# Performance work log

Measured on AMD Instinct MI355X. Metric: run time of the kernel, lower is better.

Reference implementation:

```python
import jax, jax.numpy as jnp
import numpy as np

N = 45056      # 2048 instances * 22 machines
E = 720896     # avg degree 16
FEA = 60       # max_num*6
HID = 256
MACH = 22
NEG_SLOPE = 0.01


def setup_inputs() -> dict:
    key = jax.random.key(0)
    ks = jax.random.split(key, 20)
    x = jax.random.normal(ks[0], (N, FEA), dtype=jnp.float32)
    edge_index = jax.random.randint(ks[1], (2, E), 0, N, dtype=jnp.int64)
    edge_weight = jax.random.uniform(ks[2], (E,), dtype=jnp.float32)

    def lin(k, fan_in, fan_out):
        s = 1.0 / np.sqrt(fan_in)
        kw, kb = jax.random.split(k)
        W = jax.random.uniform(kw, (fan_in, fan_out), minval=-s, maxval=s, dtype=jnp.float32)
        b = jax.random.uniform(kb, (fan_out,), minval=-s, maxval=s, dtype=jnp.float32)
        return W, b

    W1, b1 = lin(ks[3], FEA, HID)
    W2, b2 = lin(ks[4], HID, HID)
    mlp_in = MACH * (HID + FEA)  # 6952
    Wf0, bf0 = lin(ks[5], mlp_in, HID)
    Wf1, bf1 = lin(ks[6], HID, HID)
    Wf2, bf2 = lin(ks[7], HID, HID)
    Wo, bo = lin(ks[8], HID, 4)
    return {"x": x, "edge_index": edge_index, "edge_weight": edge_weight,
            "W1": W1, "b1": b1, "W2": W2, "b2": b2,
            "Wf0": Wf0, "bf0": bf0, "Wf1": Wf1, "bf1": bf1,
            "Wf2": Wf2, "bf2": bf2, "Wo": Wo, "bo": bo}


def _gcn_conv(h, W, b, row, col, norm, n):
    # h' = scatter_add(norm * (hW)[row] -> col) + b   (PyG GCNConv)
    hw = h @ W                                  # [N, out]
    msg = hw[row] * norm[:, None]               # [E+N, out]
    out = jax.ops.segment_sum(msg, col, num_segments=n)
    return out + b


def reference(x, edge_index, edge_weight, W1, b1, W2, b2,
              Wf0, bf0, Wf1, bf1, Wf2, bf2, Wo, bo):
    n = x.shape[0]
    # gcn_norm with self-loops (fill_value=1.0), symmetric normalization
    loop = jnp.arange(n, dtype=edge_index.dtype)
    row = jnp.concatenate([edge_index[0], loop])
    col = jnp.concatenate([edge_index[1], loop])
    ew = jnp.concatenate([edge_weight, jnp.ones((n,), dtype=edge_weight.dtype)])
    deg = jax.ops.segment_sum(ew, col, num_segments=n)
    dinv = jnp.where(deg > 0, jax.lax.rsqrt(jnp.maximum(deg, 1e-12)), 0.0)
    norm = dinv[row] * ew * dinv[col]

    h = _gcn_conv(x, W1, b1, row, col, norm, n)
    h = jax.nn.leaky_relu(h, NEG_SLOPE)
    # dropout p=0.5 is identity in eval mode
    h = _gcn_conv(h, W2, b2, row, col, norm, n)
    h = jax.nn.leaky_relu(h, NEG_SLOPE)

    h = jnp.concatenate([h, x], axis=1)         # [N, HID+FEA]
    flat = h.reshape(n // MACH, -1)             # [B, 22*(HID+FEA)]

    z = jax.nn.leaky_relu(flat @ Wf0 + bf0, NEG_SLOPE)
    z = jax.nn.leaky_relu(z @ Wf1 + bf1, NEG_SLOPE)
    z = jax.nn.leaky_relu(z @ Wf2 + bf2, NEG_SLOPE)
    return z @ Wo + bo                           # [B, 4]
```

## Files before the change

kernel.cpp:

```cpp
#include <hip/hip_runtime.h>
#include <stdint.h>

#define FEA 60
#define HID 256
#define MACH 22
#define PERM 316
#define PERM2 320
#define FLATP2 (MACH * PERM2)
#define NEG 0.01f

typedef __bf16 bf16x8 __attribute__((ext_vector_type(8)));
typedef float f32x4 __attribute__((ext_vector_type(4)));

__device__ __forceinline__ float bf2f(uint16_t u) {
    return __uint_as_float(((uint32_t)u) << 16);
}
__device__ __forceinline__ uint16_t f2bf(float f) {
    uint32_t x = __float_as_uint(f);
    return (uint16_t)((x + 0x7fffu + ((x >> 16) & 1u)) >> 16);
}
__device__ __forceinline__ int load_idx(const void* p, long i, int i64) {
    return i64 ? (int)((const long long*)p)[i] : ((const int*)p)[i];
}
__device__ __forceinline__ float load_w(const void* p, long i, int isbf) {
    return isbf ? bf2f(((const uint16_t*)p)[i]) : ((const float*)p)[i];
}

__global__ void k_detect(const uint32_t* ew_w, const uint32_t* ei_w, int* flags) {
    __shared__ int c15, onz;
    if (threadIdx.x == 0) { c15 = 0; onz = 0; }
    __syncthreads();
    int a = 0, b = 0;
    for (int i = threadIdx.x; i < 1024; i += 256) {
        if (ew_w[i] & 0x8000u) a++;
        if (ei_w[2 * i + 1] != 0u) b++;
    }
    atomicAdd(&c15, a); atomicAdd(&onz, b);
    __syncthreads();
    if (threadIdx.x == 0) {
        flags[0] = (c15 <= 100) ? 1 : 0;
        flags[1] = (onz < 8) ? 1 : 0;
    }
}

struct Cvt8 {
    const void* src[8];
    float* dst[8];
    long prefix[9];
    int cnt;
};

__global__ void k_cvt_f32(Cvt8 a, const int* flags) {
    int isbf = flags[0];
    long total = a.prefix[a.cnt];
    for (long i = (long)blockIdx.x * blockDim.x + threadIdx.x; i < total;
         i += (long)gridDim.x * blockDim.x) {
        int t = 0;
        while (i >= a.prefix[t + 1]) t++;
        long j = i - a.prefix[t];
        a.dst[t][j] = isbf ? bf2f(((const uint16_t*)a.src[t])[j])
                           : ((const float*)a.src[t])[j];
    }
}

__global__ void k_cvt_x(const void* src, uint16_t* dst, int n, const int* flags) {
    int isbf = flags[0];
    long total = (long)n * 64;
    for (long i = (long)blockIdx.x * blockDim.x + threadIdx.x; i < total;
         i += (long)gridDim.x * blockDim.x) {
        int col = (int)(i & 63);
        long row = i >> 6;
        uint16_t v = 0;
        if (col < FEA) {
            long s = row * FEA + col;
            v = isbf ? ((const uint16_t*)src)[s] : f2bf(((const float*)src)[s]);
        }
        dst[i] = v;
    }
}

__global__ void k_transp(const void* W, uint16_t* Wt, int K, int Kpad, const int* flags) {
    __shared__ uint16_t s[64][65];
    int isbf = flags[0];
    int k0 = blockIdx.x * 64, n0 = blockIdx.y * 64;
    int t = threadIdx.x;
#pragma unroll
    for (int i = 0; i < 16; i++) {
        int idx = t + i * 256;
        int kk = idx >> 6, nn = idx & 63;
        int k = k0 + kk;
        uint16_t v = 0;
        if (k < K) {
            long off = (long)k * HID + n0 + nn;
            v = isbf ? ((const uint16_t*)W)[off] : f2bf(((const float*)W)[off]);
        }
        s[kk][nn] = v;
    }
    __syncthreads();
#pragma unroll
    for (int i = 0; i < 16; i++) {
        int idx = t + i * 256;
        int nn = idx >> 6, kk = idx & 63;
        Wt[(long)(n0 + nn) * Kpad + k0 + kk] = s[kk][nn];
    }
}

__global__ void k_transp_wf0(const void* W, uint16_t* Wt, const int* flags) {
    __shared__ uint16_t s[64][65];
    int isbf = flags[0];
    int g0 = blockIdx.x * 64, n0 = blockIdx.y * 64;
    int t = threadIdx.x;
#pragma unroll
    for (int i = 0; i < 16; i++) {
        int idx = t + i * 256;
        int gg = idx >> 6, nn = idx & 63;
        int gk = g0 + gg;
        int m = gk / PERM2;
        int k2 = gk - m * PERM2;
        uint16_t v = 0;
        if (k2 < PERM) {
            long off = (long)(m * PERM + k2) * HID + n0 + nn;
            v = isbf ? ((const uint16_t*)W)[off] : f2bf(((const float*)W)[off]);
        }
        s[gg][nn] = v;
    }
    __syncthreads();
#pragma unroll
    for (int i = 0; i < 16; i++) {
        int idx = t + i * 256;
        int nn = idx >> 6, gg = idx & 63;
        Wt[(long)(n0 + nn) * FLATP2 + g0 + gg] = s[gg][nn];
    }
}

__global__ void k_init(int* count, int n) {
    int i = blockIdx.x * blockDim.x + threadIdx.x;
    if (i < n) count[i] = 0;
}

__global__ void k_count(const void* ei, int E, int* count, int* rank, const int* flags) {
    int e = blockIdx.x * blockDim.x + threadIdx.x;
    if (e >= E) return;
    int c = load_idx(ei, (long)E + e, flags[1]);
    rank[e] = atomicAdd(&count[c], 1);
}

__global__ void k_scan1(const int* count, int* rowptr, int* bsum, int n) {
    __shared__ int sd[1024];
    int i = blockIdx.x * 1024 + threadIdx.x;
    int v = (i < n) ? count[i] : 0;
    sd[threadIdx.x] = v;
    __syncthreads();
    for (int off = 1; off < 1024; off <<= 1) {
        int t = (threadIdx.x >= (unsigned)off) ? sd[threadIdx.x - off] : 0;
        __syncthreads();
        sd[threadIdx.x] += t;
        __syncthreads();
    }
    if (i < n) rowptr[i] = sd[threadIdx.x] - v;
    if (threadIdx.x == 1023) bsum[blockIdx.x] = sd[1023];
}

__global__ void k_scan2(int* bsum, int* boffs, int* rowptr, int nb, int n) {
    int acc = 0;
    for (int i = 0; i < nb; i++) { boffs[i] = acc; acc += bsum[i]; }
    rowptr[n] = acc;
}

__global__ void k_scan3(int* rowptr, const int* boffs, int n) {
    int i = blockIdx.x * 1024 + threadIdx.x;
    if (i < n) rowptr[i] += boffs[blockIdx.x];
}

__global__ void k_fill(const void* ei, const void* ew, const int* rowptr, const int* rank,
                       int* adj_src, float* adj_w, int E, const int* flags) {
    int e = blockIdx.x * blockDim.x + threadIdx.x;
    if (e >= E) return;
    int i64 = flags[1];
    int r = load_idx(ei, e, i64);
    int c = load_idx(ei, (long)E + e, i64);
    float w = load_w(ew, e, flags[0]);
    int pos = rowptr[c] + rank[e];
    adj_src[pos] = r;
    adj_w[pos] = w;
}

__global__ void k_rowsum(const int* rowptr, const float* adj_w, float* dinv, int n) {
    int i = blockIdx.x * blockDim.x + threadIdx.x;
    if (i >= n) return;
    int s = rowptr[i], e = rowptr[i + 1];
    double d = 1.0;
    for (int p = s; p < e; p++) d += (double)adj_w[p];
    dinv[i] = (float)(1.0 / sqrt(d));
}

__global__ __launch_bounds__(256) void k_aggx(const uint16_t* __restrict__ x64,
                                              const float* __restrict__ dinv,
                                              const int* __restrict__ rowptr,
                                              const int* __restrict__ adj_src,
                                              const float* __restrict__ adj_w,
                                              uint16_t* __restrict__ xa, int n) {
    __shared__ int ssrc[8][32];
    __shared__ float swt[8][32];
    int hwv = threadIdx.x >> 5;
    int l32 = threadIdx.x & 31;
    int node = blockIdx.x * 8 + hwv;
    if (node >= n) return;
    const uint32_t* xu = (const uint32_t*)x64;
    float di = dinv[node];
    float c2 = di * di;
    uint32_t h = xu[(long)node * 32 + l32];
    float a0 = c2 * bf2f((uint16_t)(h & 0xffff));
    float a1 = c2 * bf2f((uint16_t)(h >> 16));
    int s = rowptr[node], e = rowptr[node + 1];
    for (int base = s; base < e; base += 32) {
        int m = e - base; if (m > 32) m = 32;
        if (l32 < m) {
            int s0 = adj_src[base + l32];
            ssrc[hwv][l32] = s0;
            swt[hwv][l32] = adj_w[base + l32] * dinv[s0] * di;
        }
        for (int t = 0; t < m; t++) {
            int src = ssrc[hwv][t];
            float w = swt[hwv][t];
            uint32_t v = xu[(long)src * 32 + l32];
            a0 += w * bf2f((uint16_t)(v & 0xffff));
            a1 += w * bf2f((uint16_t)(v >> 16));
        }
    }
    ((uint32_t*)xa)[(long)node * 32 + l32] =
        (uint32_t)f2bf(a0) | ((uint32_t)f2bf(a1) << 16);
}

__global__ __launch_bounds__(256) void k_aggb(const uint16_t* __restrict__ hw,
                                              const float* __restrict__ dinv,
                                              const int* __restrict__ rowptr,
                                              const int* __restrict__ adj_src,
                                              const float* __restrict__ adj_w,
                                              const float* __restrict__ bias,
                                              uint16_t* __restrict__ out, int n) {
    __shared__ int ssrc[4][64];
    __shared__ float swt[4][64];
    int wv = threadIdx.x >> 6;
    int lane = threadIdx.x & 63;
    int node = blockIdx.x * 4 + wv;
    if (node >= n) return;
    const uint2* hw2 = (const uint2*)hw;
    float di = dinv[node];
    float c2 = di * di;
    uint2 h = hw2[(long)node * 64 + lane];
    float a0 = c2 * bf2f((uint16_t)(h.x & 0xffff));
    float a1 = c2 * bf2f((uint16_t)(h.x >> 16));
    float a2 = c2 * bf2f((uint16_t)(h.y & 0xffff));
    float a3 = c2 * bf2f((uint16_t)(h.y >> 16));
    int s = rowptr[node], e = rowptr[node + 1];
    for (int base = s; base < e; base += 64) {
        int m = e - base; if (m > 64) m = 64;
        if (lane < m) {
            int s0 = adj_src[base + lane];
            ssrc[wv][lane] = s0;
            swt[wv][lane] = adj_w[base + lane] * dinv[s0] * di;
        }
        for (int t = 0; t < m; t++) {
            int src = ssrc[wv][t];
            float w = swt[wv][t];
            uint2 v = hw2[(long)src * 64 + lane];
            a0 += w * bf2f((uint16_t)(v.x & 0xffff));
            a1 += w * bf2f((uint16_t)(v.x >> 16));
            a2 += w * bf2f((uint16_t)(v.y & 0xffff));
            a3 += w * bf2f((uint16_t)(v.y >> 16));
        }
    }
    float4 b4 = ((const float4*)bias)[lane];
    a0 += b4.x; a1 += b4.y; a2 += b4.z; a3 += b4.w;
    a0 = a0 > 0.f ? a0 : NEG * a0;
    a1 = a1 > 0.f ? a1 : NEG * a1;
    a2 = a2 > 0.f ? a2 : NEG * a2;
    a3 = a3 > 0.f ? a3 : NEG * a3;
    uint2 o;
    o.x = (uint32_t)f2bf(a0) | ((uint32_t)f2bf(a1) << 16);
    o.y = (uint32_t)f2bf(a2) | ((uint32_t)f2bf(a3) << 16);
    ((uint2*)out)[(long)node * 64 + lane] = o;
}

__global__ __launch_bounds__(256) void k_mgemm(const uint16_t* __restrict__ A,
                                               const uint16_t* __restrict__ Bt,
                                               float* __restrict__ part,
                                               uint16_t* __restrict__ outb,
                                               const float* __restrict__ bias,
                                               int M, int K, int Kc, int act) {
    __shared__ uint16_t As[128 * 40];
    __shared__ uint16_t Bs[128 * 40];
    int tid = threadIdx.x;
    int lane = tid & 63, wv = tid >> 6;
    int quad = lane >> 4, l15 = lane & 15;
    int row0 = blockIdx.y * 128, col0 = blockIdx.x * 128;
    int kbeg = blockIdx.z * Kc;
    int kend = kbeg + Kc; if (kend > K) kend = K;
    int arow = (wv >> 1) * 64;
    int bcol = (wv & 1) * 64;

    f32x4 acc[4][4];
#pragma unroll
    for (int i = 0; i < 4; i++)
#pragma unroll
        for (int j = 0; j < 4; j++) acc[i][j] = (f32x4){0.f, 0.f, 0.f, 0.f};

    for (int kc = kbeg; kc < kend; kc += 32) {
#pragma unroll
        for (int i = 0; i < 2; i++) {
            int idx = tid + i * 256;
            int r = idx >> 2, cq = idx & 3;
            uint4 va = *(const uint4*)(A + (long)(row0 + r) * K + kc + cq * 8);
            *(uint4*)(&As[r * 40 + cq * 8]) = va;
            uint4 vb = *(const uint4*)(Bt + (long)(col0 + r) * K + kc + cq * 8);
            *(uint4*)(&Bs[r * 40 + cq * 8]) = vb;
        }
        __syncthreads();
        bf16x8 af[4], bfr[4];
#pragma unroll
        for (int i = 0; i < 4; i++)
            af[i] = __builtin_bit_cast(bf16x8,
                *(const uint4*)(&As[(arow + i * 16 + l15) * 40 + quad * 8]));
#pragma unroll
        for (int j = 0; j < 4; j++)
            bfr[j] = __builtin_bit_cast(bf16x8,
                *(const uint4*)(&Bs[(bcol + j * 16 + l15) * 40 + quad * 8]));
#pragma unroll
        for (int i = 0; i < 4; i++)
#pragma unroll
            for (int j = 0; j < 4; j++)
                acc[i][j] = __builtin_amdgcn_mfma_f32_16x16x32_bf16(af[i], bfr[j], acc[i][j], 0, 0, 0);
        __syncthreads();
    }

#pragma unroll
    for (int i = 0; i < 4; i++)
#pragma unroll
        for (int j = 0; j < 4; j++) {
            int row = row0 + arow + i * 16 + quad * 4;
            int col = col0 + bcol + j * 16 + l15;
#pragma unroll
            for (int reg = 0; reg < 4; reg++) {
                float v = acc[i][j][reg];
                long o = (long)(row + reg) * HID + col;
                if (part) part[(long)blockIdx.z * M * HID + o] = v;
                else {
                    if (bias) v += bias[col];
                    if (act) v = v > 0.f ? v : NEG * v;
                    outb[o] = f2bf(v);
                }
            }
        }
}

__global__ __launch_bounds__(256) void k_mgemm_flat(const uint16_t* __restrict__ h2,
                                                    const uint16_t* __restrict__ x64,
                                                    const uint16_t* __restrict__ Bt,
                                                    float* __restrict__ part,
                                                    int M, int Kc) {
    __shared__ uint16_t As[128 * 40];
    __shared__ uint16_t Bs[128 * 40];
    int tid = threadIdx.x;
    int lane = tid & 63, wv = tid >> 6;
    int quad = lane >> 4, l15 = lane & 15;
    int row0 = blockIdx.y * 128, col0 = blockIdx.x * 128;
    int kbeg = blockIdx.z * Kc;
    int kend = kbeg + Kc;
    int arow = (wv >> 1) * 64;
    int bcol = (wv & 1) * 64;

    f32x4 acc[4][4];
#pragma unroll
    for (int i = 0; i < 4; i++)
#pragma unroll
        for (int j = 0; j < 4; j++) acc[i][j] = (f32x4){0.f, 0.f, 0.f, 0.f};

    for (int kc = kbeg; kc < kend; kc += 32) {
#pragma unroll
        for (int i = 0; i < 2; i++) {
            int idx = tid + i * 256;
            int r = idx >> 2, cq = idx & 3;
            int gk = kc + cq * 8;
            int m = gk / PERM2;
            int k2 = gk - m * PERM2;
            long node = (long)(row0 + r) * MACH + m;
            uint4 va = (k2 < HID)
                ? *(const uint4*)(h2 + node * HID + k2)
                : *(const uint4*)(x64 + node * 64 + (k2 - HID));
            *(uint4*)(&As[r * 40 + cq * 8]) = va;
            uint4 vb = *(const uint4*)(Bt + (long)(col0 + r) * FLATP2 + gk);
            *(uint4*)(&Bs[r * 40 + cq * 8]) = vb;
        }
        __syncthreads();
        bf16x8 af[4], bfr[4];
#pragma unroll
        for (int i = 0; i < 4; i++)
            af[i] = __builtin_bit_cast(bf16x8,
                *(const uint4*)(&As[(arow + i * 16 + l15) * 40 + quad * 8]));
#pragma unroll
        for (int j = 0; j < 4; j++)
            bfr[j] = __builtin_bit_cast(bf16x8,
                *(const uint4*)(&Bs[(bcol + j * 16 + l15) * 40 + quad * 8]));
#pragma unroll
        for (int i = 0; i < 4; i++)
#pragma unroll
            for (int j = 0; j < 4; j++)
                acc[i][j] = __builtin_amdgcn_mfma_f32_16x16x32_bf16(af[i], bfr[j], acc[i][j], 0, 0, 0);
        __syncthreads();
    }

#pragma unroll
    for (int i = 0; i < 4; i++)
#pragma unroll
        for (int j = 0; j < 4; j++) {
            int row = row0 + arow + i * 16 + quad * 4;
            int col = col0 + bcol + j * 16 + l15;
#pragma unroll
            for (int reg = 0; reg < 4; reg++)
                part[(long)blockIdx.z * M * HID + (long)(row + reg) * HID + col] = acc[i][j][reg];
        }
}

__global__ void k_reduce(const float* __restrict__ part, const float* __restrict__ bias,
                         uint16_t* __restrict__ out, int MN, int S) {
    int i = blockIdx.x * blockDim.x + threadIdx.x;
    if (i >= MN) return;
    float v = 0.f;
    for (int s = 0; s < S; s++) v += part[(long)s * MN + i];
    v += bias[i & (HID - 1)];
    v = v > 0.f ? v : NEG * v;
    out[i] = f2bf(v);
}

__global__ __launch_bounds__(256) void k_tail(const uint16_t* __restrict__ z0,
                                              const uint16_t* __restrict__ Wf1t,
                                              const float* __restrict__ bf1,
                                              const uint16_t* __restrict__ Wf2t,
                                              const float* __restrict__ bf2,
                                              const float* __restrict__ Wo,
                                              const float* __restrict__ bo,
                                              void* out, const int* flags) {
    __shared__ uint16_t z1s[16 * 256];
    __shared__ uint16_t z2s[16 * 256];
    int tid = threadIdx.x;
    int lane = tid & 63, wv = tid >> 6;
    int quad = lane >> 4, l15 = lane & 15;
    int rows0 = blockIdx.x * 16;
    int nw = wv * 64;

    {
        f32x4 acc[4];
#pragma unroll
        for (int j = 0; j < 4; j++) acc[j] = (f32x4){0.f, 0.f, 0.f, 0.f};
        for (int kc = 0; kc < HID; kc += 32) {
            bf16x8 a = __builtin_bit_cast(bf16x8,
                *(const uint4*)(z0 + (long)(rows0 + l15) * HID + kc + quad * 8));
#pragma unroll
            for (int j = 0; j < 4; j++) {
                bf16x8 b = __builtin_bit_cast(bf16x8,
                    *(const uint4*)(Wf1t + (long)(nw + j * 16 + l15) * HID + kc + quad * 8));
                acc[j] = __builtin_amdgcn_mfma_f32_16x16x32_bf16(a, b, acc[j], 0, 0, 0);
            }
        }
#pragma unroll
        for (int j = 0; j < 4; j++) {
            int col = nw + j * 16 + l15;
            float bj = bf1[col];
#pragma unroll
            for (int reg = 0; reg < 4; reg++) {
                float v = acc[j][reg] + bj;
                v = v > 0.f ? v : NEG * v;
                z1s[(quad * 4 + reg) * 256 + col] = f2bf(v);
            }
        }
    }
    __syncthreads();

    {
        f32x4 acc[4];
#pragma unroll
        for (int j = 0; j < 4; j++) acc[j] = (f32x4){0.f, 0.f, 0.f, 0.f};
        for (int kc = 0; kc < HID; kc += 32) {
            bf16x8 a = __builtin_bit_cast(bf16x8,
                *(const uint4*)(&z1s[l15 * 256 + kc + quad * 8]));
#pragma unroll
            for (int j = 0; j < 4; j++) {
                bf16x8 b = __builtin_bit_cast(bf16x8,
                    *(const uint4*)(Wf2t + (long)(nw + j * 16 + l15) * HID + kc + quad * 8));
                acc[j] = __builtin_amdgcn_mfma_f32_16x16x32_bf16(a, b, acc[j], 0, 0, 0);
            }
        }
#pragma unroll
        for (int j = 0; j < 4; j++) {
            int col = nw + j * 16 + l15;
            float bj = bf2[col];
#pragma unroll
            for (int reg = 0; reg < 4; reg++) {
                float v = acc[j][reg] + bj;
                v = v > 0.f ? v : NEG * v;
                z2s[(quad * 4 + reg) * 256 + col] = f2bf(v);
            }
        }
    }
    __syncthreads();

    if (tid < 64) {
        int r = tid >> 2, o = tid & 3;
        float acc = bo[o];
        for (int k = 0; k < HID; k++)
            acc += bf2f(z2s[r * 256 + k]) * Wo[k * 4 + o];
        long idx = (long)(rows0 + r) * 4 + o;
        if (flags[0]) ((uint16_t*)out)[idx] = f2bf(acc);
        else          ((float*)out)[idx] = acc;
    }
}

extern "C" void kernel_launch(void* const* d_in, const int* in_sizes, int n_in,
                              void* d_out, int out_size, void* d_ws, size_t ws_size,
                              hipStream_t stream) {
    const int N  = in_sizes[0] / FEA;
    const int E  = in_sizes[2];
    const int Bn = N / MACH;
    const int S0 = 11, Kc0 = FLATP2 / 11;

    char* ws = (char*)d_ws;
    size_t off = 0;
    auto alloc = [&](size_t bytes) -> char* {
        char* p = ws + off;
        off = (off + bytes + 255) & ~(size_t)255;
        return p;
    };

    int*      flags  = (int*)     alloc(64);
    uint16_t* x64    = (uint16_t*)alloc((size_t)N * 64 * 2);
    uint16_t* xa     = (uint16_t*)alloc((size_t)N * 64 * 2);
    uint16_t* W1t    = (uint16_t*)alloc((size_t)HID * 64 * 2);
    uint16_t* W2t    = (uint16_t*)alloc((size_t)HID * HID * 2);
    uint16_t* Wf0t   = (uint16_t*)alloc((size_t)HID * FLATP2 * 2);
    uint16_t* Wf1t   = (uint16_t*)alloc((size_t)HID * HID * 2);
    uint16_t* Wf2t   = (uint16_t*)alloc((size_t)HID * HID * 2);
    float*    b1     = (float*)   alloc(HID * 4);
    float*    b2     = (float*)   alloc(HID * 4);
    float*    bf0    = (float*)   alloc(HID * 4);
    float*    bf1    = (float*)   alloc(HID * 4);
    float*    bf2    = (float*)   alloc(HID * 4);
    float*    Wo     = (float*)   alloc((size_t)HID * 4 * 4);
    float*    bo     = (float*)   alloc(4 * 4);
    int*      count  = (int*)     alloc((size_t)N * 4);
    int*      rank   = (int*)     alloc((size_t)E * 4);
    int*      rowptr = (int*)     alloc((size_t)(N + 1) * 4);
    int*      bsum   = (int*)     alloc(64 * 4);
    int*      boffs  = (int*)     alloc(64 * 4);
    int*      adj_src= (int*)     alloc((size_t)E * 4);
    float*    adj_w  = (float*)   alloc((size_t)E * 4);
    float*    dinv   = (float*)   alloc((size_t)N * 4);
    uint16_t* P      = (uint16_t*)alloc((size_t)N * HID * 2);
    uint16_t* Q      = (uint16_t*)alloc((size_t)N * HID * 2);
    float*    part   = (float*)   alloc((size_t)S0 * Bn * HID * 4);
    uint16_t* z0     = (uint16_t*)alloc((size_t)Bn * HID * 2);
    (void)ws_size; (void)n_in; (void)out_size;

    k_detect<<<1, 256, 0, stream>>>((const uint32_t*)d_in[2], (const uint32_t*)d_in[1], flags);

    Cvt8 c8{};
    const void* s8[7] = { d_in[4], d_in[6], d_in[8], d_in[10], d_in[12], d_in[13], d_in[14] };
    float* d8[7] = { b1, b2, bf0, bf1, bf2, Wo, bo };
    long n8[7] = { HID, HID, HID, HID, HID, (long)HID * 4, 4 };
    c8.cnt = 7;
    c8.prefix[0] = 0;
    for (int t = 0; t < 7; t++) { c8.src[t] = s8[t]; c8.dst[t] = d8[t]; c8.prefix[t + 1] = c8.prefix[t] + n8[t]; }
    c8.prefix[8] = c8.prefix[7];
    k_cvt_f32<<<64, 256, 0, stream>>>(c8, flags);
    k_cvt_x<<<2048, 256, 0, stream>>>(d_in[0], x64, N, flags);
    k_transp<<<dim3(1, 4), 256, 0, stream>>>(d_in[3], W1t, FEA, 64, flags);
    k_transp<<<dim3(4, 4), 256, 0, stream>>>(d_in[5], W2t, HID, HID, flags);
    k_transp_wf0<<<dim3(FLATP2 / 64, 4), 256, 0, stream>>>(d_in[7], Wf0t, flags);
    k_transp<<<dim3(4, 4), 256, 0, stream>>>(d_in[9], Wf1t, HID, HID, flags);
    k_transp<<<dim3(4, 4), 256, 0, stream>>>(d_in[11], Wf2t, HID, HID, flags);

    k_init<<<(N + 255) / 256, 256, 0, stream>>>(count, N);
    k_count<<<(E + 255) / 256, 256, 0, stream>>>(d_in[1], E, count, rank, flags);
    int nb = (N + 1023) / 1024;
    k_scan1<<<nb, 1024, 0, stream>>>(count, rowptr, bsum, N);
    k_scan2<<<1, 1, 0, stream>>>(bsum, boffs, rowptr, nb, N);
    k_scan3<<<nb, 1024, 0, stream>>>(rowptr, boffs, N);
    k_fill<<<(E + 255) / 256, 256, 0, stream>>>(d_in[1], d_in[2], rowptr, rank, adj_src, adj_w, E, flags);
    k_rowsum<<<(N + 255) / 256, 256, 0, stream>>>(rowptr, adj_w, dinv, N);

    k_aggx<<<(N + 7) / 8, 256, 0, stream>>>(x64, dinv, rowptr, adj_src, adj_w, xa, N);
    k_mgemm<<<dim3(2, N / 128, 1), 256, 0, stream>>>(xa, W1t, nullptr, P, b1, N, 64, 64, 1);

    k_mgemm<<<dim3(2, N / 128, 1), 256, 0, stream>>>(P, W2t, nullptr, Q, nullptr, N, HID, HID, 0);
    k_aggb<<<(N + 3) / 4, 256, 0, stream>>>(Q, dinv, rowptr, adj_src, adj_w, b2, P, N);

    k_mgemm_flat<<<dim3(2, Bn / 128, S0), 256, 0, stream>>>(P, x64, Wf0t, part, Bn, Kc0);
    k_reduce<<<(Bn * HID + 255) / 256, 256, 0, stream>>>(part, bf0, z0, Bn * HID, S0);

    k_tail<<<Bn / 16, 256, 0, stream>>>(z0, Wf1t, bf1, Wf2t, bf2, Wo, bo, d_out, flags);
}
```

Baseline: 374.2 us.

## Fuse setup kernels, pack adjacency as uint2, widen gather loads and retune split-K

Merges several small preprocessing launches (detect+init, x and bias conversion, three weight transposes, scan2 into scan3) to cut launch overhead. Packs the CSR source index and weight into a single uint2 array and processes two edges per thread in count/fill. The aggregation kernels get 4-way unrolled gathers, and k_aggb switches to 32-lane half-waves with 16-byte loads. The split-K for the first flat GEMM changes from 11 to 8 splits with clamping. Risks include more serial prefix work in scan3 and fewer workgroups in the flat GEMM.

```diff
diff --git a/kernel.cpp b/kernel.cpp
--- a/kernel.cpp
+++ b/kernel.cpp
@@ -19,27 +19,26 @@
     uint32_t x = __float_as_uint(f);
     return (uint16_t)((x + 0x7fffu + ((x >> 16) & 1u)) >> 16);
 }
-__device__ __forceinline__ int load_idx(const void* p, long i, int i64) {
-    return i64 ? (int)((const long long*)p)[i] : ((const int*)p)[i];
-}
-__device__ __forceinline__ float load_w(const void* p, long i, int isbf) {
-    return isbf ? bf2f(((const uint16_t*)p)[i]) : ((const float*)p)[i];
-}
-
-__global__ void k_detect(const uint32_t* ew_w, const uint32_t* ei_w, int* flags) {
-    __shared__ int c15, onz;
-    if (threadIdx.x == 0) { c15 = 0; onz = 0; }
-    __syncthreads();
-    int a = 0, b = 0;
-    for (int i = threadIdx.x; i < 1024; i += 256) {
-        if (ew_w[i] & 0x8000u) a++;
-        if (ei_w[2 * i + 1] != 0u) b++;
-    }
-    atomicAdd(&c15, a); atomicAdd(&onz, b);
-    __syncthreads();
-    if (threadIdx.x == 0) {
-        flags[0] = (c15 <= 100) ? 1 : 0;
-        flags[1] = (onz < 8) ? 1 : 0;
+
+__global__ void k_detect_init(const uint32_t* ew_w, const uint32_t* ei_w, int* flags,
+                              int* count, int n) {
+    int i = blockIdx.x * blockDim.x + threadIdx.x;
+    if (i < n) count[i] = 0;
+    if (blockIdx.x == 0) {
+        __shared__ int c15, onz;
+        if (threadIdx.x == 0) { c15 = 0; onz = 0; }
+        __syncthreads();
+        int a = 0, b = 0;
+        for (int k = threadIdx.x; k < 1024; k += 256) {
+            if (ew_w[k] & 0x8000u) a++;
+            if (ei_w[2 * k + 1] != 0u) b++;
+        }
+        atomicAdd(&c15, a); atomicAdd(&onz, b);
+        __syncthreads();
+        if (threadIdx.x == 0) {
+            flags[0] = (c15 <= 100) ? 1 : 0;
+            flags[1] = (onz < 8) ? 1 : 0;
+        }
     }
 }
 
@@ -50,32 +49,29 @@
     int cnt;
 };
 
-__global__ void k_cvt_f32(Cvt8 a, const int* flags) {
+__global__ void k_cvt_all(const void* xsrc, uint16_t* x64, int n, Cvt8 a, const int* flags) {
     int isbf = flags[0];
-    long total = a.prefix[a.cnt];
+    long nx = (long)n * 64;
+    long total = nx + a.prefix[a.cnt];
     for (long i = (long)blockIdx.x * blockDim.x + threadIdx.x; i < total;
          i += (long)gridDim.x * blockDim.x) {
-        int t = 0;
-        while (i >= a.prefix[t + 1]) t++;
-        long j = i - a.prefix[t];
-        a.dst[t][j] = isbf ? bf2f(((const uint16_t*)a.src[t])[j])
-                           : ((const float*)a.src[t])[j];
-    }
-}
-
-__global__ void k_cvt_x(const void* src, uint16_t* dst, int n, const int* flags) {
-    int isbf = flags[0];
-    long total = (long)n * 64;
-    for (long i = (long)blockIdx.x * blockDim.x + threadIdx.x; i < total;
-         i += (long)gridDim.x * blockDim.x) {
-        int col = (int)(i & 63);
-        long row = i >> 6;
-        uint16_t v = 0;
-        if (col < FEA) {
-            long s = row * FEA + col;
-            v = isbf ? ((const uint16_t*)src)[s] : f2bf(((const float*)src)[s]);
-        }
-        dst[i] = v;
+        if (i < nx) {
+            int col = (int)(i & 63);
+            long row = i >> 6;
+            uint16_t v = 0;
+            if (col < FEA) {
+                long s = row * FEA + col;
+                v = isbf ? ((const uint16_t*)xsrc)[s] : f2bf(((const float*)xsrc)[s]);
+            }
+            x64[i] = v;
+        } else {
+            long ii = i - nx;
+            int t = 0;
+            while (ii >= a.prefix[t + 1]) t++;
+            long j = ii - a.prefix[t];
+            a.dst[t][j] = isbf ? bf2f(((const uint16_t*)a.src[t])[j])
+                               : ((const float*)a.src[t])[j];
+        }
     }
 }
 
@@ -102,6 +98,30 @@
         int idx = t + i * 256;
         int nn = idx >> 6, kk = idx & 63;
         Wt[(long)(n0 + nn) * Kpad + k0 + kk] = s[kk][nn];
+    }
+}
+
+struct T3 { const void* src[3]; uint16_t* dst[3]; };
+__global__ void k_transp3(T3 a, const int* flags) {
+    __shared__ uint16_t s[64][65];
+    int isbf = flags[0];
+    const void* W = a.src[blockIdx.z];
+    uint16_t* Wt = a.dst[blockIdx.z];
+    int k0 = blockIdx.x * 64, n0 = blockIdx.y * 64;
+    int t = threadIdx.x;
+#pragma unroll
+    for (int i = 0; i < 16; i++) {
+        int idx = t + i * 256;
+        int kk = idx >> 6, nn = idx & 63;
+        long off = (long)(k0 + kk) * HID + n0 + nn;
+        s[kk][nn] = isbf ? ((const uint16_t*)W)[off] : f2bf(((const float*)W)[off]);
+    }
+    __syncthreads();
+#pragma unroll
+    for (int i = 0; i < 16; i++) {
+        int idx = t + i * 256;
+        int nn = idx >> 6, kk = idx & 63;
+        Wt[(long)(n0 + nn) * HID + k0 + kk] = s[kk][nn];
     }
 }
 
@@ -133,16 +153,22 @@
     }
 }
 
-__global__ void k_init(int* count, int n) {
-    int i = blockIdx.x * blockDim.x + threadIdx.x;
-    if (i < n) count[i] = 0;
-}
-
 __global__ void k_count(const void* ei, int E, int* count, int* rank, const int* flags) {
-    int e = blockIdx.x * blockDim.x + threadIdx.x;
-    if (e >= E) return;
-    int c = load_idx(ei, (long)E + e, flags[1]);
-    rank[e] = atomicAdd(&count[c], 1);
+    int e0 = (blockIdx.x * blockDim.x + threadIdx.x) * 2;
+    if (e0 >= E) return;
+    int i64 = flags[1];
+    int c0, c1 = -1;
+    if (i64) {
+        const long long* p = (const long long*)ei + E + e0;
+        c0 = (int)p[0];
+        if (e0 + 1 < E) c1 = (int)p[1];
+    } else {
+        const int* p = (const int*)ei + E + e0;
+        c0 = p[0];
+        if (e0 + 1 < E) c1 = p[1];
+    }
+    rank[e0] = atomicAdd(&count[c0], 1);
+    if (c1 >= 0) rank[e0 + 1] = atomicAdd(&count[c1], 1);
 }
 
 __global__ void k_scan1(const int* count, int* rowptr, int* bsum, int n) {
@@ -161,126 +187,188 @@
     if (threadIdx.x == 1023) bsum[blockIdx.x] = sd[1023];
 }
 
-__global__ void k_scan2(int* bsum, int* boffs, int* rowptr, int nb, int n) {
-    int acc = 0;
-    for (int i = 0; i < nb; i++) { boffs[i] = acc; acc += bsum[i]; }
-    rowptr[n] = acc;
-}
-
-__global__ void k_scan3(int* rowptr, const int* boffs, int n) {
+__global__ void k_scan3(int* rowptr, const int* bsum, int nb, int n) {
+    __shared__ int sboff;
+    if (threadIdx.x == 0) {
+        int acc = 0;
+        for (int i = 0; i < (int)blockIdx.x; i++) acc += bsum[i];
+        sboff = acc;
+        if ((int)blockIdx.x == nb - 1) rowptr[n] = acc + bsum[nb - 1];
+    }
+    __syncthreads();
     int i = blockIdx.x * 1024 + threadIdx.x;
-    if (i < n) rowptr[i] += boffs[blockIdx.x];
+    if (i < n) rowptr[i] += sboff;
 }
 
 __global__ void k_fill(const void* ei, const void* ew, const int* rowptr, const int* rank,
-                       int* adj_src, float* adj_w, int E, const int* flags) {
-    int e = blockIdx.x * blockDim.x + threadIdx.x;
-    if (e >= E) return;
-    int i64 = flags[1];
-    int r = load_idx(ei, e, i64);
-    int c = load_idx(ei, (long)E + e, i64);
-    float w = load_w(ew, e, flags[0]);
-    int pos = rowptr[c] + rank[e];
-    adj_src[pos] = r;
-    adj_w[pos] = w;
-}
-
-__global__ void k_rowsum(const int* rowptr, const float* adj_w, float* dinv, int n) {
+                       uint2* adj, int E, const int* flags) {
+    int e0 = (blockIdx.x * blockDim.x + threadIdx.x) * 2;
+    if (e0 >= E) return;
+    int i64 = flags[1], isbf = flags[0];
+    int r0, r1 = -1, c0, c1 = -1;
+    if (i64) {
+        const long long* pr = (const long long*)ei + e0;
+        const long long* pc = (const long long*)ei + E + e0;
+        r0 = (int)pr[0]; c0 = (int)pc[0];
+        if (e0 + 1 < E) { r1 = (int)pr[1]; c1 = (int)pc[1]; }
+    } else {
+        const int* pr = (const int*)ei + e0;
+        const int* pc = (const int*)ei + E + e0;
+        r0 = pr[0]; c0 = pc[0];
+        if (e0 + 1 < E) { r1 = pr[1]; c1 = pc[1]; }
+    }
+    float w0, w1 = 0.f;
+    if (isbf) {
+        uint32_t ww = ((const uint32_t*)ew)[e0 >> 1];
+        w0 = bf2f((uint16_t)(ww & 0xffff));
+        w1 = bf2f((uint16_t)(ww >> 16));
+    } else {
+        float2 f = ((const float2*)ew)[e0 >> 1];
+        w0 = f.x; w1 = f.y;
+    }
+    int2 rk = *(const int2*)(rank + e0);
+    uint2 v0; v0.x = (uint32_t)r0; v0.y = __float_as_uint(w0);
+    adj[rowptr[c0] + rk.x] = v0;
+    if (c1 >= 0) {
+        uint2 v1; v1.x = (uint32_t)r1; v1.y = __float_as_uint(w1);
+        adj[rowptr[c1] + rk.y] = v1;
+    }
+}
+
+__global__ void k_rowsum(const int* rowptr, const uint2* adj, float* dinv, int n) {
     int i = blockIdx.x * blockDim.x + threadIdx.x;
     if (i >= n) return;
     int s = rowptr[i], e = rowptr[i + 1];
     double d = 1.0;
-    for (int p = s; p < e; p++) d += (double)adj_w[p];
+    for (int p = s; p < e; p++) d += (double)__uint_as_float(adj[p].y);
     dinv[i] = (float)(1.0 / sqrt(d));
 }
 
 __global__ __launch_bounds__(256) void k_aggx(const uint16_t* __restrict__ x64,
                                               const float* __restrict__ dinv,
                                               const int* __restrict__ rowptr,
-                                              const int* __restrict__ adj_src,
-                                              const float* __restrict__ adj_w,
+                                              const uint2* __restrict__ adj,
                                               uint16_t* __restrict__ xa, int n) {
-    __shared__ int ssrc[8][32];
-    __shared__ float swt[8][32];
-    int hwv = threadIdx.x >> 5;
-    int l32 = threadIdx.x & 31;
-    int node = blockIdx.x * 8 + hwv;
+    __shared__ uint2 sadj[8][32];
+    int hv = threadIdx.x >> 5;
+    int l = threadIdx.x & 31;
+    int node = blockIdx.x * 8 + hv;
     if (node >= n) return;
     const uint32_t* xu = (const uint32_t*)x64;
     float di = dinv[node];
     float c2 = di * di;
-    uint32_t h = xu[(long)node * 32 + l32];
+    uint32_t h = xu[(long)node * 32 + l];
     float a0 = c2 * bf2f((uint16_t)(h & 0xffff));
     float a1 = c2 * bf2f((uint16_t)(h >> 16));
     int s = rowptr[node], e = rowptr[node + 1];
     for (int base = s; base < e; base += 32) {
         int m = e - base; if (m > 32) m = 32;
-        if (l32 < m) {
-            int s0 = adj_src[base + l32];
-            ssrc[hwv][l32] = s0;
-            swt[hwv][l32] = adj_w[base + l32] * dinv[s0] * di;
-        }
-        for (int t = 0; t < m; t++) {
-            int src = ssrc[hwv][t];
-            float w = swt[hwv][t];
-            uint32_t v = xu[(long)src * 32 + l32];
-            a0 += w * bf2f((uint16_t)(v & 0xffff));
-            a1 += w * bf2f((uint16_t)(v >> 16));
-        }
-    }
-    ((uint32_t*)xa)[(long)node * 32 + l32] =
+        if (l < m) {
+            uint2 a = adj[base + l];
+            float w = __uint_as_float(a.y) * dinv[a.x] * di;
+            uint2 p; p.x = a.x; p.y = __float_as_uint(w);
+            sadj[hv][l] = p;
+        }
+        int t = 0;
+        for (; t + 4 <= m; t += 4) {
+            uint2 e0 = sadj[hv][t], e1 = sadj[hv][t + 1], e2 = sadj[hv][t + 2], e3 = sadj[hv][t + 3];
+            uint32_t v0 = xu[(long)e0.x * 32 + l];
+            uint32_t v1 = xu[(long)e1.x * 32 + l];
+            uint32_t v2 = xu[(long)e2.x * 32 + l];
+            uint32_t v3 = xu[(long)e3.x * 32 + l];
+            float w0 = __uint_as_float(e0.y), w1 = __uint_as_float(e1.y);
+            float w2 = __uint_as_float(e2.y), w3 = __uint_as_float(e3.y);
+            a0 += w0 * bf2f((uint16_t)(v0 & 0xffff)); a1 += w0 * bf2f((uint16_t)(v0 >> 16));
+            a0 += w1 * bf2f((uint16_t)(v1 & 0xffff)); a1 += w1 * bf2f((uint16_t)(v1 >> 16));
+            a0 += w2 * bf2f((uint16_t)(v2 & 0xffff)); a1 += w2 * bf2f((uint16_t)(v2 >> 16));
+            a0 += w3 * bf2f((uint16_t)(v3 & 0xffff)); a1 += w3 * bf2f((uint16_t)(v3 >> 16));
+        }
+        for (; t < m; t++) {
+            uint2 e0 = sadj[hv][t];
+            uint32_t v0 = xu[(long)e0.x * 32 + l];
+            float w0 = __uint_as_float(e0.y);
+            a0 += w0 * bf2f((uint16_t)(v0 & 0xffff));
+            a1 += w0 * bf2f((uint16_t)(v0 >> 16));
+        }
+    }
+    ((uint32_t*)xa)[(long)node * 32 + l] =
         (uint32_t)f2bf(a0) | ((uint32_t)f2bf(a1) << 16);
+}
+
+__device__ __forceinline__ void fma8(float* acc, float w, uint4 v) {
+    acc[0] += w * bf2f((uint16_t)(v.x & 0xffff));
+    acc[1] += w * bf2f((uint16_t)(v.x >> 16));
+    acc[2] += w * bf2f((uint16_t)(v.y & 0xffff));
+    acc[3] += w * bf2f((uint16_t)(v.y >> 16));
+    acc[4] += w * bf2f((uint16_t)(v.z & 0xffff));
+    acc[5] += w * bf2f((uint16_t)(v.z >> 16));
+    acc[6] += w * bf2f((uint16_t)(v.w & 0xffff));
+    acc[7] += w * bf2f((uint16_t)(v.w >> 16));
 }
 
 __global__ __launch_bounds__(256) void k_aggb(const uint16_t* __restrict__ hw,
                                               const float* __restrict__ dinv,
                                               const int* __restrict__ rowptr,
-                                              const int* __restrict__ adj_src,
-                                              const float* __restrict__ adj_w,
+                                              const uint2* __restrict__ adj,
                                               const float* __restrict__ bias,
                                               uint16_t* __restrict__ out, int n) {
-    __shared__ int ssrc[4][64];
-    __shared__ float swt[4][64];
-    int wv = threadIdx.x >> 6;
-    int lane = threadIdx.x & 63;
-    int node = blockIdx.x * 4 + wv;
+    __shared__ uint2 sadj[8][32];
+    int hv = threadIdx.x >> 5;
+    int l = threadIdx.x & 31;
+    int node = blockIdx.x * 8 + hv;
     if (node >= n) return;
-    const uint2* hw2 = (const uint2*)hw;
+    const uint4* hw4 = (const uint4*)hw;
     float di = dinv[node];
     float c2 = di * di;
-    uint2 h = hw2[(long)node * 64 + lane];
-    float a0 = c2 * bf2f((uint16_t)(h.x & 0xffff));
-    float a1 = c2 * bf2f((uint16_t)(h.x >> 16));
-    float a2 = c2 * bf2f((uint16_t)(h.y & 0xffff));
-    float a3 = c2 * bf2f((uint16_t)(h.y >> 16));
+    uint4 h = hw4[(long)node * 32 + l];
+    float acc[8];
+    acc[0] = c2 * bf2f((uint16_t)(h.x & 0xffff));
+    acc[1] = c2 * bf2f((uint16_t)(h.x >> 16));
+    acc[2] = c2 * bf2f((uint16_t)(h.y & 0xffff));
+    acc[3] = c2 * bf2f((uint16_t)(h.y >> 16));
+    acc[4] = c2 * bf2f((uint16_t)(h.z & 0xffff));
+    acc[5] = c2 * bf2f((uint16_t)(h.z >> 16));
+    acc[6] = c2 * bf2f((uint16_t)(h.w & 0xffff));
+    acc[7] = c2 * bf2f((uint16_t)(h.w >> 16));
     int s = rowptr[node], e = rowptr[node + 1];
-    for (int base = s; base < e; base += 64) {
-        int m = e - base; if (m > 64) m = 64;
-        if (lane < m) {
-            int s0 = adj_src[base + lane];
-            ssrc[wv][lane] = s0;
-            swt[wv][lane] = adj_w[base + lane] * dinv[s0] * di;
-        }
-        for (int t = 0; t < m; t++) {
-            int src = ssrc[wv][t];
-            float w = swt[wv][t];
-            uint2 v = hw2[(long)src * 64 + lane];
-            a0 += w * bf2f((uint16_t)(v.x & 0xffff));
-            a1 += w * bf2f((uint16_t)(v.x >> 16));
-            a2 += w * bf2f((uint16_t)(v.y & 0xffff));
-            a3 += w * bf2f((uint16_t)(v.y >> 16));
-        }
-    }
-    float4 b4 = ((const float4*)bias)[lane];
-    a0 += b4.x; a1 += b4.y; a2 += b4.z; a3 += b4.w;
-    a0 = a0 > 0.f ? a0 : NEG * a0;
-    a1 = a1 > 0.f ? a1 : NEG * a1;
-    a2 = a2 > 0.f ? a2 : NEG * a2;
-    a3 = a3 > 0.f ? a3 : NEG * a3;
-    uint2 o;
-    o.x = (uint32_t)f2bf(a0) | ((uint32_t)f2bf(a1) << 16);
-    o.y = (uint32_t)f2bf(a2) | ((uint32_t)f2bf(a3) << 16);
-    ((uint2*)out)[(long)node * 64 + lane] = o;
+    for (int base = s; base < e; base += 32) {
+        int m = e - base; if (m > 32) m = 32;
+        if (l < m) {
+            uint2 a = adj[base + l];
+            float w = __uint_as_float(a.y) * dinv[a.x] * di;
+            uint2 p; p.x = a.x; p.y = __float_as_uint(w);
+            sadj[hv][l] = p;
+        }
+        int t = 0;
+        for (; t + 4 <= m; t += 4) {
+            uint2 e0 = sadj[hv][t], e1 = sadj[hv][t + 1], e2 = sadj[hv][t + 2], e3 = sadj[hv][t + 3];
+            uint4 v0 = hw4[(long)e0.x * 32 + l];
+            uint4 v1 = hw4[(long)e1.x * 32 + l];
+            uint4 v2 = hw4[(long)e2.x * 32 + l];
+            uint4 v3 = hw4[(long)e3.x * 32 + l];
+            fma8(acc, __uint_as_float(e0.y), v0);
+            fma8(acc, __uint_as_float(e1.y), v1);
+            fma8(acc, __uint_as_float(e2.y), v2);
+            fma8(acc, __uint_as_float(e3.y), v3);
+        }
+        for (; t < m; t++) {
+            uint2 e0 = sadj[hv][t];
+            uint4 v0 = hw4[(long)e0.x * 32 + l];
+            fma8(acc, __uint_as_float(e0.y), v0);
+        }
+    }
+    float4 ba = ((const float4*)bias)[l * 2];
+    float4 bb = ((const float4*)bias)[l * 2 + 1];
+    acc[0] += ba.x; acc[1] += ba.y; acc[2] += ba.z; acc[3] += ba.w;
+    acc[4] += bb.x; acc[5] += bb.y; acc[6] += bb.z; acc[7] += bb.w;
+#pragma unroll
+    for (int k = 0; k < 8; k++) acc[k] = acc[k] > 0.f ? acc[k] : NEG * acc[k];
+    uint4 o;
+    o.x = (uint32_t)f2bf(acc[0]) | ((uint32_t)f2bf(acc[1]) << 16);
+    o.y = (uint32_t)f2bf(acc[2]) | ((uint32_t)f2bf(acc[3]) << 16);
+    o.z = (uint32_t)f2bf(acc[4]) | ((uint32_t)f2bf(acc[5]) << 16);
+    o.w = (uint32_t)f2bf(acc[6]) | ((uint32_t)f2bf(acc[7]) << 16);
+    ((uint4*)out)[(long)node * 32 + l] = o;
 }
 
 __global__ __launch_bounds__(256) void k_mgemm(const uint16_t* __restrict__ A,
@@ -366,7 +454,7 @@
     int quad = lane >> 4, l15 = lane & 15;
     int row0 = blockIdx.y * 128, col0 = blockIdx.x * 128;
     int kbeg = blockIdx.z * Kc;
-    int kend = kbeg + Kc;
+    int kend = kbeg + Kc; if (kend > FLATP2) kend = FLATP2;
     int arow = (wv >> 1) * 64;
     int bcol = (wv & 1) * 64;
 
@@ -522,7 +610,7 @@
     const int N  = in_sizes[0] / FEA;
     const int E  = in_sizes[2];
     const int Bn = N / MACH;
-    const int S0 = 11, Kc0 = FLATP2 / 11;
+    const int S0 = 8, Kc0 = 896;
 
     char* ws = (char*)d_ws;
     size_t off = 0;
@@ -551,9 +639,7 @@
     int*      rank   = (int*)     alloc((size_t)E * 4);
     int*      rowptr = (int*)     alloc((size_t)(N + 1) * 4);
     int*      bsum   = (int*)     alloc(64 * 4);
-    int*      boffs  = (int*)     alloc(64 * 4);
-    int*      adj_src= (int*)     alloc((size_t)E * 4);
-    float*    adj_w  = (float*)   alloc((size_t)E * 4);
+    uint2*    adj    = (uint2*)   alloc((size_t)E * 8);
     float*    dinv   = (float*)   alloc((size_t)N * 4);
     uint16_t* P      = (uint16_t*)alloc((size_t)N * HID * 2);
     uint16_t* Q      = (uint16_t*)alloc((size_t)N * HID * 2);
@@ -561,7 +647,8 @@
     uint16_t* z0     = (uint16_t*)alloc((size_t)Bn * HID * 2);
     (void)ws_size; (void)n_in; (void)out_size;
 
-    k_detect<<<1, 256, 0, stream>>>((const uint32_t*)d_in[2], (const uint32_t*)d_in[1], flags);
+    k_detect_init<<<(N + 255) / 256, 256, 0, stream>>>(
+        (const uint32_t*)d_in[2], (const uint32_t*)d_in[1], flags, count, N);
 
     Cvt8 c8{};
     const void* s8[7] = { d_in[4], d_in[6], d_in[8], d_in[10], d_in[12], d_in[13], d_in[14] };
@@ -571,28 +658,27 @@
     c8.prefix[0] = 0;
     for (int t = 0; t < 7; t++) { c8.src[t] = s8[t]; c8.dst[t] = d8[t]; c8.prefix[t + 1] = c8.prefix[t] + n8[t]; }
     c8.prefix[8] = c8.prefix[7];
-    k_cvt_f32<<<64, 256, 0, stream>>>(c8, flags);
-    k_cvt_x<<<2048, 256, 0, stream>>>(d_in[0], x64, N, flags);
+    k_cvt_all<<<2048, 256, 0, stream>>>(d_in[0], x64, N, c8, flags);
     k_transp<<<dim3(1, 4), 256, 0, stream>>>(d_in[3], W1t, FEA, 64, flags);
-    k_transp<<<dim3(4, 4), 256, 0, stream>>>(d_in[5], W2t, HID, HID, flags);
+    T3 t3{};
+    t3.src[0] = d_in[5];  t3.dst[0] = W2t;
+    t3.src[1] = d_in[9];  t3.dst[1] = Wf1t;
+    t3.src[2] = d_in[11]; t3.dst[2] = Wf2t;
+    k_transp3<<<dim3(4, 4, 3), 256, 0, stream>>>(t3, flags);
     k_transp_wf0<<<dim3(FLATP2 / 64, 4), 256, 0, stream>>>(d_in[7], Wf0t, flags);
-    k_transp<<<dim3(4, 4), 256, 0, stream>>>(d_in[9], Wf1t, HID, HID, flags);
-    k_transp<<<dim3(4, 4), 256, 0, stream>>>(d_in[11], Wf2t, HID, HID, flags);
-
-    k_init<<<(N + 255) / 256, 256, 0, stream>>>(count, N);
-    k_count<<<(E + 255) / 256, 256, 0, stream>>>(d_in[1], E, count, rank, flags);
+
+    k_count<<<(E / 2 + 255) / 256, 256, 0, stream>>>(d_in[1], E, count, rank, flags);
     int nb = (N + 1023) / 1024;
     k_scan1<<<nb, 1024, 0, stream>>>(count, rowptr, bsum, N);
-    k_scan2<<<1, 1, 0, stream>>>(bsum, boffs, rowptr, nb, N);
-    k_scan3<<<nb, 1024, 0, stream>>>(rowptr, boffs, N);
-    k_fill<<<(E + 255) / 256, 256, 0, stream>>>(d_in[1], d_in[2], rowptr, rank, adj_src, adj_w, E, flags);
-    k_rowsum<<<(N + 255) / 256, 256, 0, stream>>>(rowptr, adj_w, dinv, N);
-
-    k_aggx<<<(N + 7) / 8, 256, 0, stream>>>(x64, dinv, rowptr, adj_src, adj_w, xa, N);
+    k_scan3<<<nb, 1024, 0, stream>>>(rowptr, bsum, nb, N);
+    k_fill<<<(E / 2 + 255) / 256, 256, 0, stream>>>(d_in[1], d_in[2], rowptr, rank, adj, E, flags);
+    k_rowsum<<<(N + 255) / 256, 256, 0, stream>>>(rowptr, adj, dinv, N);
+
+    k_aggx<<<(N + 7) / 8, 256, 0, stream>>>(x64, dinv, rowptr, adj, xa, N);
     k_mgemm<<<dim3(2, N / 128, 1), 256, 0, stream>>>(xa, W1t, nullptr, P, b1, N, 64, 64, 1);
 
     k_mgemm<<<dim3(2, N / 128, 1), 256, 0, stream>>>(P, W2t, nullptr, Q, nullptr, N, HID, HID, 0);
-    k_aggb<<<(N + 3) / 4, 256, 0, stream>>>(Q, dinv, rowptr, adj_src, adj_w, b2, P, N);
+    k_aggb<<<(N + 7) / 8, 256, 0, stream>>>(Q, dinv, rowptr, adj, b2, P, N);
 
     k_mgemm_flat<<<dim3(2, Bn / 128, S0), 256, 0, stream>>>(P, x64, Wf0t, part, Bn, Kc0);
     k_reduce<<<(Bn * HID + 255) / 256, 256, 0, stream>>>(part, bf0, z0, Bn * HID, S0);
```

Result: faster. 344.1 us (-8.0%).
